# Kernel tuning notes

Measured on AMD Instinct MI355X. Metric: run time of the kernel, lower is better.

## Reference

```python
import jax, jax.numpy as jnp
import numpy as np

D_MODEL, D_STATE, D_CONV, EXPAND = 1024, 16, 4, 2
D_INNER = EXPAND * D_MODEL
B, L = 2, 2048


def setup_inputs() -> dict:
    key = jax.random.key(0)
    ks = jax.random.split(key, 8)
    s = lambda fan: 1.0 / np.sqrt(fan)
    x = jax.random.normal(ks[0], (B, L, D_MODEL), dtype=jnp.float32)
    W_in = jax.random.normal(ks[1], (2 * D_INNER, D_MODEL), dtype=jnp.float32) * s(D_MODEL)
    conv_w = jax.random.normal(ks[2], (D_INNER, 1, D_CONV), dtype=jnp.float32) * s(D_CONV)
    conv_b = jax.random.normal(ks[3], (D_INNER,), dtype=jnp.float32) * 0.01
    A_log = jnp.log(jnp.abs(jax.random.normal(ks[4], (D_INNER, D_STATE), dtype=jnp.float32)) + 1e-4)
    Dp = jnp.ones((D_INNER,), dtype=jnp.float32)
    W_dt = jax.random.normal(ks[5], (D_INNER, D_INNER), dtype=jnp.float32) * s(D_INNER)
    b_dt = jax.random.normal(ks[6], (D_INNER,), dtype=jnp.float32) * 0.01
    W_out = jax.random.normal(ks[7], (D_MODEL, D_INNER), dtype=jnp.float32) * s(D_INNER)
    return {"x": x, "W_in": W_in, "conv_w": conv_w, "conv_b": conv_b,
            "A_log": A_log, "Dp": Dp, "W_dt": W_dt, "b_dt": b_dt, "W_out": W_out}


def _mamba_fwd(x, W_in, conv_w, conv_b, A_log, Dp, W_dt, b_dt, W_out):
    Bsz, Ln, _ = x.shape
    xz = x @ W_in.T                                  # [B, L, 2*d_inner]
    x_proj, z = jnp.split(xz, 2, axis=-1)            # each [B, L, d_inner]
    # depthwise causal conv1d: left-pad d_conv-1 (matches torch pad + [:L] slice)
    xc = jnp.transpose(x_proj, (0, 2, 1))            # [B, C, L]
    xc = jax.lax.conv_general_dilated(
        xc, conv_w, window_strides=(1,), padding=[(D_CONV - 1, 0)],
        dimension_numbers=("NCH", "OIH", "NCH"), feature_group_count=D_INNER)
    xc = xc + conv_b[None, :, None]
    x_act = jax.nn.silu(jnp.transpose(xc, (0, 2, 1)))  # [B, L, d_inner]
    dt = jax.nn.softplus(x_act @ W_dt.T + b_dt)        # [B, L, d_inner]
    A = -jnp.exp(A_log)                                # [d_inner, d_state]

    def step(h, inp):
        xt, dt_t = inp                                 # [B, d_inner] each
        dA = jnp.exp(dt_t[:, :, None] * A[None])       # [B, d_inner, d_state]
        dB = (dt_t * xt)[:, :, None]                   # broadcast over states
        h = dA * h + dB
        y_t = h.sum(axis=-1) + Dp * xt                 # [B, d_inner]
        return h, y_t

    h0 = jnp.zeros((Bsz, D_INNER, D_STATE), dtype=x.dtype)
    xs = (jnp.transpose(x_act, (1, 0, 2)), jnp.transpose(dt, (1, 0, 2)))  # [L, B, d_inner]
    _, ys = jax.lax.scan(step, h0, xs)
    y_ssm = jnp.transpose(ys, (1, 0, 2))               # [B, L, d_inner]
    y_gated = y_ssm * jax.nn.silu(z)
    return y_gated @ W_out.T                           # [B, L, d_model]


def reference(x, W_in, conv_w, conv_b, A_log, Dp, W_dt, b_dt, W_out):
    return _mamba_fwd(x, W_in, conv_w, conv_b, A_log, Dp, W_dt, b_dt, W_out)
```

## Files before the change

### kernel.cpp

```cpp
#include <hip/hip_runtime.h>

#define DMODEL 1024
#define DSTATE 16
#define DCONV  4
#define DINNER 2048
#define BSZ    2
#define LSEQ   2048
#define MTOT   (BSZ * LSEQ)
#define NCH    64
#define LC     (LSEQ / NCH)
#define LOG2E  1.44269504088896f

typedef unsigned short u16;
typedef __attribute__((ext_vector_type(8))) short short8;
typedef __attribute__((ext_vector_type(8))) unsigned short u16x8;
typedef __attribute__((ext_vector_type(4))) float f32x4;

__device__ __forceinline__ float silu_f(float v) {
  return v * __builtin_amdgcn_rcpf(1.f + __builtin_amdgcn_exp2f(-v * LOG2E));
}

__device__ __forceinline__ u16 f2bf(float f) {
  unsigned int u = __float_as_uint(f);
  u += 0x7FFF + ((u >> 16) & 1);
  return (u16)(u >> 16);
}
__device__ __forceinline__ float bf2f(u16 b) { return __uint_as_float(((unsigned int)b) << 16); }

__device__ __forceinline__ void gload_lds16(const u16* g, u16* l) {
  __builtin_amdgcn_global_load_lds((const __attribute__((address_space(1))) unsigned int*)g,
                                   (__attribute__((address_space(3))) unsigned int*)l, 16, 0, 0);
}

__global__ __launch_bounds__(256)
void cast4(const float4* __restrict__ s0, ushort4* __restrict__ d0, int n0,
           const float4* __restrict__ s1, ushort4* __restrict__ d1, int n1,
           const float4* __restrict__ s2, ushort4* __restrict__ d2, int n2,
           const float4* __restrict__ s3, ushort4* __restrict__ d3, int n3) {
  int i = blockIdx.x * 256 + threadIdx.x;
  const float4* s; ushort4* d;
  if (i < n0)                { s = s0; d = d0; }
  else if ((i -= n0) < n1)   { s = s1; d = d1; }
  else if ((i -= n1) < n2)   { s = s2; d = d2; }
  else if ((i -= n2) < n3)   { s = s3; d = d3; }
  else return;
  float4 v = s[i];
  ushort4 o = { f2bf(v.x), f2bf(v.y), f2bf(v.z), f2bf(v.w) };
  d[i] = o;
}

template<int BN, int MODE, int OBF>
__global__ __launch_bounds__(512, 2)
void gemm8p(const u16* __restrict__ A, const u16* __restrict__ Bm,
            const float* __restrict__ bias, void* __restrict__ Cv,
            int M, int N, int K) {
  constexpr int BT  = BN / 32;
  constexpr int TJP = 2;
  constexpr int NPH = BT / TJP;
  constexpr int NBH = BN / 128;
  extern __shared__ __align__(16) u16 smem[];
  u16* As = smem;
  u16* Bs = smem + 2 * 256 * 64;

  const int tid  = threadIdx.x;
  const int lane = tid & 63;
  const int w    = tid >> 6;
  const int quad = lane >> 4;
  const int l16  = lane & 15;
  const int wm   = (w >> 1) * 64;
  const int wn   = (w & 1) * (BN / 2);

  const int nbn = N / BN, nbm = M >> 8;
  const int pid = blockIdx.x;
  const int npg = 4 * nbn;
  const int fm  = (pid / npg) * 4;
  const int gsz = (nbm - fm < 4) ? (nbm - fm) : 4;
  const int bm  = (fm + (pid % gsz)) << 8;
  const int bn  = ((pid % npg) / gsz) * BN;

  const int rseg = lane >> 3;
  const int cd8  = (((lane & 7) ^ rseg) << 3);
  const u16* gA = A  + (size_t)(bm + 16 * w + rseg) * K + cd8;
  const u16* gB = Bm + (size_t)(bn + 16 * w + rseg) * K + cd8;
  u16* lA = &As[(2 * w) << 9];
  u16* lB = &Bs[(2 * w) << 9];
  const int Kmask = K - 1;

  auto stA = [&](int slot, int h, int kt) {
    const size_t go = (size_t)h * 128 * K + ((kt << 6) & Kmask);
    gload_lds16(gA + go,         lA + slot * 16384 + h * 8192);
    gload_lds16(gA + go + 8 * K, lA + slot * 16384 + h * 8192 + 512);
  };
  auto stB = [&](int slot, int h, int kt) {
    const size_t go = (size_t)h * 128 * K + ((kt << 6) & Kmask);
    gload_lds16(gB + go,         lB + slot * (BN * 64) + h * 8192);
    gload_lds16(gB + go + 8 * K, lB + slot * (BN * 64) + h * 8192 + 512);
  };

  int aoff[4][2], boff[BT][2];
#pragma unroll
  for (int t = 0; t < 4; ++t) {
    const int ra = wm + 16 * t + l16;
#pragma unroll
    for (int ks = 0; ks < 2; ++ks)
      aoff[t][ks] = ra * 64 + (((quad + 4 * ks) ^ (ra & 7)) << 3);
  }
#pragma unroll
  for (int tj = 0; tj < BT; ++tj) {
    const int rb = wn + 16 * tj + l16;
#pragma unroll
    for (int ks = 0; ks < 2; ++ks)
      boff[tj][ks] = rb * 64 + (((quad + 4 * ks) ^ (rb & 7)) << 3);
  }

  f32x4 acc[4][BT] = {};
  short8 af[4][2];

#define RD_AF(slot)                                                          \
  { _Pragma("unroll") for (int t = 0; t < 4; ++t)                            \
      _Pragma("unroll") for (int ks = 0; ks < 2; ++ks)                       \
        af[t][ks] = *(const short8*)&As[(slot) * 16384 + aoff[t][ks]]; }

#define VM4 asm volatile("s_waitcnt vmcnt(4)" ::: "memory")
#define NOWAIT ((void)0)

#define PHASE(slot, j, STG, WAIT)                                            \
  {                                                                          \
    if ((j) == 0) RD_AF(slot);                                               \
    short8 bfp[TJP][2];                                                      \
    _Pragma("unroll") for (int jj = 0; jj < TJP; ++jj)                       \
      _Pragma("unroll") for (int ks = 0; ks < 2; ++ks)                       \
        bfp[jj][ks] = *(const short8*)&Bs[(slot) * (BN * 64) +               \
                                          boff[(j) * TJP + jj][ks]];         \
    STG;                                                                     \
    __builtin_amdgcn_s_setprio(1);                                           \
    _Pragma("unroll") for (int ks = 0; ks < 2; ++ks)                         \
      _Pragma("unroll") for (int jj = 0; jj < TJP; ++jj)                     \
        _Pragma("unroll") for (int t = 0; t < 4; ++t)                        \
          acc[t][(j) * TJP + jj] = __builtin_amdgcn_mfma_f32_16x16x32_bf16(  \
              af[t][ks], bfp[jj][ks], acc[t][(j) * TJP + jj], 0, 0, 0);      \
    __builtin_amdgcn_s_setprio(0);                                           \
    asm volatile("s_waitcnt lgkmcnt(0)" ::: "memory");                       \
    WAIT;                                                                    \
    __builtin_amdgcn_s_barrier();                                            \
  }

  stA(0, 0, 0); stA(0, 1, 0);
  stB(0, 0, 0); if (NBH == 2) stB(0, 1, 0);
  stA(1, 0, 1); stA(1, 1, 1);
  VM4;
  __builtin_amdgcn_s_barrier();

  const int niter = K >> 7;
  for (int i = 0; i < niter; ++i) {
    const int tb1 = 2 * i + 1, t2 = 2 * i + 2, t3 = 2 * i + 3;
    if constexpr (NPH == 4) {
      PHASE(0, 0, { stB(1, 0, tb1); },               NOWAIT);
      PHASE(0, 1, { stB(1, 1, tb1); stA(0, 0, t2); }, NOWAIT);
      PHASE(0, 2, { stA(0, 1, t2); },                NOWAIT);
      PHASE(0, 3, {},                                VM4);
      PHASE(1, 0, { stB(0, 0, t2); },                NOWAIT);
      PHASE(1, 1, { stB(0, 1, t2); stA(1, 0, t3); }, NOWAIT);
      PHASE(1, 2, { stA(1, 1, t3); },                NOWAIT);
      PHASE(1, 3, {},                                VM4);
    } else {
      PHASE(0, 0, { stB(1, 0, tb1); },                NOWAIT);
      PHASE(0, 1, { stA(0, 0, t2); stA(0, 1, t2); },  VM4);
      PHASE(1, 0, { stB(0, 0, t2); },                 NOWAIT);
      PHASE(1, 1, { stA(1, 0, t3); stA(1, 1, t3); },  VM4);
    }
  }
#undef PHASE
#undef RD_AF
#undef VM4
#undef NOWAIT

  asm volatile("s_waitcnt vmcnt(0)" ::: "memory");

  const bool dosilu = (MODE == 2) && (bn >= (N >> 1));
#pragma unroll
  for (int t = 0; t < 4; ++t) {
    const int row0 = bm + wm + 16 * t + quad * 4;
#pragma unroll
    for (int tj = 0; tj < BT; ++tj) {
      const int col = bn + wn + 16 * tj + l16;
      const float bv = (MODE == 1) ? bias[col] : 0.f;
#pragma unroll
      for (int i2 = 0; i2 < 4; ++i2) {
        float v = acc[t][tj][i2] + bv;
        if (MODE == 1) v = (v > 20.f) ? v : __logf(1.f + __expf(v));
        if (MODE == 2 && dosilu) v = silu_f(v);
        if (OBF) ((u16*)Cv)[(size_t)(row0 + i2) * N + col] = f2bf(v);
        else     ((float*)Cv)[(size_t)(row0 + i2) * N + col] = v;
      }
    }
  }
}

template<int MODE, int OBF, int BN>
__global__ __launch_bounds__(256)
void hgemm_bk128(const u16* __restrict__ A, const u16* __restrict__ B,
                 const float* __restrict__ bias, void* __restrict__ Cv,
                 int M, int N, int K) {
  constexpr int ASEG = 32;
  constexpr int BSEG = BN / 4;
  constexpr int SPW  = (ASEG + BSEG) / 4;
  constexpr int BT   = BN / 32;
  __shared__ u16 As[128 * 128];
  __shared__ u16 Bs[BN * 128];
  const int tid  = threadIdx.x;
  const int lane = tid & 63;
  const int w    = tid >> 6;
  const int quad = lane >> 4;
  const int l16  = lane & 15;

  const int nbn = N / BN, nbm = M >> 7;
  const int pid = blockIdx.x;
  const int npg = 4 * nbn;
  const int fm  = (pid / npg) * 4;
  const int gsz = (nbm - fm < 4) ? (nbm - fm) : 4;
  const int bm  = (fm + (pid % gsz)) << 7;
  const int bn  = ((pid % npg) / gsz) * BN;

  const int wm = (w & 1) * 64;
  const int wn = (w >> 1) * (BN / 2);

  const int rs4 = lane >> 4;
  const u16* Gp[SPW]; u16* Lp[SPW];
#pragma unroll
  for (int q = 0; q < SPW; ++q) {
    const int g = w * SPW + q;
    if (g < ASEG) {
      const int r  = g * 4 + rs4;
      const int cdk = (lane & 15) ^ (r & 15);
      Gp[q] = A + (size_t)(bm + r) * K + (cdk << 3);
      Lp[q] = &As[g << 9];
    } else {
      const int r  = (g - ASEG) * 4 + rs4;
      const int cdk = (lane & 15) ^ (r & 15);
      Gp[q] = B + (size_t)(bn + r) * K + (cdk << 3);
      Lp[q] = &Bs[(g - ASEG) << 9];
    }
  }

  const short8* Afp[4][4];
  const short8* Bfp[BT][4];
#pragma unroll
  for (int t = 0; t < 4; ++t) {
    const int ra = wm + 16 * t + l16;
#pragma unroll
    for (int ks = 0; ks < 4; ++ks)
      Afp[t][ks] = (const short8*)&As[ra * 128 + (((quad + 4 * ks) ^ (ra & 15)) << 3)];
  }
#pragma unroll
  for (int t = 0; t < BT; ++t) {
    const int rb = wn + 16 * t + l16;
#pragma unroll
    for (int ks = 0; ks < 4; ++ks)
      Bfp[t][ks] = (const short8*)&Bs[rb * 128 + (((quad + 4 * ks) ^ (rb & 15)) << 3)];
  }

  f32x4 acc[4][BT] = {};

  for (int k0 = 0; k0 < K; k0 += 128) {
#pragma unroll
    for (int q = 0; q < SPW; ++q) { gload_lds16(Gp[q], Lp[q]); Gp[q] += 128; }
    __syncthreads();
#pragma unroll
    for (int ks = 0; ks < 4; ++ks) {
      short8 af[4], bf[BT];
#pragma unroll
      for (int t = 0; t < 4; ++t) af[t] = *Afp[t][ks];
#pragma unroll
      for (int t = 0; t < BT; ++t) bf[t] = *Bfp[t][ks];
#pragma unroll
      for (int ti = 0; ti < 4; ++ti)
#pragma unroll
        for (int tj = 0; tj < BT; ++tj)
          acc[ti][tj] = __builtin_amdgcn_mfma_f32_16x16x32_bf16(af[ti], bf[tj],
                                                                acc[ti][tj], 0, 0, 0);
    }
    __syncthreads();
  }

#pragma unroll
  for (int ti = 0; ti < 4; ++ti) {
    const int row0 = bm + wm + 16 * ti + quad * 4;
#pragma unroll
    for (int tj = 0; tj < BT; ++tj) {
      const int col = bn + wn + 16 * tj + l16;
      const float bv = (MODE == 1) ? bias[col] : 0.f;
#pragma unroll
      for (int i = 0; i < 4; ++i) {
        float v = acc[ti][tj][i] + bv;
        if (MODE == 1) v = (v > 20.f) ? v : __logf(1.f + __expf(v));
        if (OBF) ((u16*)Cv)[(size_t)(row0 + i) * N + col] = f2bf(v);
        else     ((float*)Cv)[(size_t)(row0 + i) * N + col] = v;
      }
    }
  }
}

__global__ __launch_bounds__(256)
void conv_silu(const u16* __restrict__ xz, const float* __restrict__ conv_w,
               const float* __restrict__ conv_b, u16* __restrict__ xact) {
  const int i  = blockIdx.x * 256 + threadIdx.x;
  const int ko = i & 255;
  const int t4 = (i >> 8) & (LSEQ / 4 - 1);
  const int b  = i >> 17;
  const int c  = ko << 3;
  const int t0 = t4 << 2;
  float wv[4][8], bias[8];
#pragma unroll
  for (int j = 0; j < 8; ++j) {
    bias[j] = conv_b[c + j];
    const float4 w4 = *(const float4*)(conv_w + (c + j) * DCONV);
    wv[0][j] = w4.x; wv[1][j] = w4.y; wv[2][j] = w4.z; wv[3][j] = w4.w;
  }
  float win[7][8];
#pragma unroll
  for (int r = 0; r < 7; ++r) {
    const int tt = t0 - 3 + r;
    if (tt >= 0) {
      const u16x8 v = *(const u16x8*)(xz + ((size_t)(b * LSEQ + tt) << 12) + c);
#pragma unroll
      for (int j = 0; j < 8; ++j) win[r][j] = bf2f(v[j]);
    } else {
#pragma unroll
      for (int j = 0; j < 8; ++j) win[r][j] = 0.f;
    }
  }
#pragma unroll
  for (int o = 0; o < 4; ++o) {
    u16x8 outv;
#pragma unroll
    for (int j = 0; j < 8; ++j) {
      float a = bias[j];
#pragma unroll
      for (int k = 0; k < 4; ++k) a = fmaf(win[o + k][j], wv[k][j], a);
      outv[j] = f2bf(silu_f(a));
    }
    *(u16x8*)(xact + ((size_t)(b * LSEQ + t0 + o) << 11) + c) = outv;
  }
}


__global__ __launch_bounds__(256, 2)
void scan_pass1(const u16* __restrict__ dtb, const u16* __restrict__ xact,
                const float* __restrict__ A_log,
                u16* __restrict__ hbuf, float* __restrict__ sumdt) {
  const int gid = blockIdx.x * 256 + threadIdx.x;
  const int c  = gid & (DINNER - 1);
  const int ch = (gid >> 11) & (NCH - 1);
  const int b  = gid >> 17;
  float a2[16];
#pragma unroll
  for (int s = 0; s < 16; ++s)
    a2[s] = -__expf(A_log[c * DSTATE + s]) * LOG2E;
  const size_t base = ((size_t)(b * LSEQ + ch * LC) << 11) + c;
  float h[16] = {};
  float sd = 0.f;
  for (int j = 0; j < LC; j += 2) {
    const float dt0 = bf2f(dtb [base + ((size_t)j << 11)]);
    const float xv0 = bf2f(xact[base + ((size_t)j << 11)]);
    const float dt1 = bf2f(dtb [base + ((size_t)(j + 1) << 11)]);
    const float xv1 = bf2f(xact[base + ((size_t)(j + 1) << 11)]);
    const float dx0 = dt0 * xv0, dx1 = dt1 * xv1;
    sd += dt0 + dt1;
#pragma unroll
    for (int s = 0; s < 16; ++s)
      h[s] = fmaf(__builtin_amdgcn_exp2f(dt0 * a2[s]), h[s], dx0);
#pragma unroll
    for (int s = 0; s < 16; ++s)
      h[s] = fmaf(__builtin_amdgcn_exp2f(dt1 * a2[s]), h[s], dx1);
  }
  u16x8* ho = (u16x8*)&hbuf[(((size_t)(b * NCH + ch) * DINNER) + c) << 4];
  u16x8 lo, hi;
#pragma unroll
  for (int s = 0; s < 8; ++s) { lo[s] = f2bf(h[s]); hi[s] = f2bf(h[8 + s]); }
  ho[0] = lo; ho[1] = hi;
  sumdt[(size_t)(b * NCH + ch) * DINNER + c] = sd;
}

__global__ __launch_bounds__(256)
void scan_combine(u16* __restrict__ hbuf, const float* __restrict__ sumdt,
                  const float* __restrict__ A_log) {
  const int gid = blockIdx.x * 256 + threadIdx.x;
  const int s = gid & 15;
  const int c = (gid >> 4) & (DINNER - 1);
  const int b = gid >> 15;
  const float a2 = -__expf(A_log[c * DSTATE + s]) * LOG2E;
  float h = 0.f;
  for (int k = 0; k < NCH; ++k) {
    const size_t o = (((size_t)(b * NCH + k) * DINNER) + c) * 16 + s;
    const float he = bf2f(hbuf[o]);
    const float sd = sumdt[(size_t)(b * NCH + k) * DINNER + c];
    hbuf[o] = f2bf(h);
    h = fmaf(__builtin_amdgcn_exp2f(sd * a2), h, he);
  }
}

__global__ __launch_bounds__(256, 2)
void scan_pass3(const u16* __restrict__ dtb, const u16* __restrict__ xact,
                const u16* __restrict__ xz, const float* __restrict__ A_log,
                const float* __restrict__ Dp, const u16* __restrict__ hbuf,
                u16* __restrict__ yg) {
  const int gid = blockIdx.x * 256 + threadIdx.x;
  const int c  = gid & (DINNER - 1);
  const int ch = (gid >> 11) & (NCH - 1);
  const int b  = gid >> 17;
  float a2[16];
#pragma unroll
  for (int s = 0; s < 16; ++s)
    a2[s] = -__expf(A_log[c * DSTATE + s]) * LOG2E;
  const float dp = Dp[c];
  float h[16];
  const u16x8* hi = (const u16x8*)&hbuf[(((size_t)(b * NCH + ch) * DINNER) + c) << 4];
  const u16x8 vlo = hi[0], vhi = hi[1];
#pragma unroll
  for (int s = 0; s < 8; ++s) { h[s] = bf2f(vlo[s]); h[8 + s] = bf2f(vhi[s]); }
  const size_t base  = ((size_t)(b * LSEQ + ch * LC) << 11) + c;
  const size_t zbase = ((size_t)(b * LSEQ + ch * LC) << 12) + DINNER + c;
  for (int j = 0; j < LC; j += 2) {
    const float dt0 = bf2f(dtb [base + ((size_t)j << 11)]);
    const float xv0 = bf2f(xact[base + ((size_t)j << 11)]);
    const float zv0 = bf2f(xz[zbase + ((size_t)j << 12)]);
    const float dt1 = bf2f(dtb [base + ((size_t)(j + 1) << 11)]);
    const float xv1 = bf2f(xact[base + ((size_t)(j + 1) << 11)]);
    const float zv1 = bf2f(xz[zbase + ((size_t)(j + 1) << 12)]);
    const float dx0 = dt0 * xv0, dx1 = dt1 * xv1;
    float y0 = 0.f, y1 = 0.f;
#pragma unroll
    for (int s = 0; s < 16; ++s) {
      h[s] = fmaf(__builtin_amdgcn_exp2f(dt0 * a2[s]), h[s], dx0);
      y0 += h[s];
    }
#pragma unroll
    for (int s = 0; s < 16; ++s) {
      h[s] = fmaf(__builtin_amdgcn_exp2f(dt1 * a2[s]), h[s], dx1);
      y1 += h[s];
    }
    y0 = fmaf(dp, xv0, y0);
    y1 = fmaf(dp, xv1, y1);
    yg[base + ((size_t)j << 11)]       = f2bf(y0 * zv0);
    yg[base + ((size_t)(j + 1) << 11)] = f2bf(y1 * zv1);
  }
}

extern "C" void kernel_launch(void* const* d_in, const int* in_sizes, int n_in,
                              void* d_out, int out_size, void* d_ws, size_t ws_size,
                              hipStream_t stream) {
  const float* x      = (const float*)d_in[0];
  const float* W_in   = (const float*)d_in[1];
  const float* conv_w = (const float*)d_in[2];
  const float* conv_b = (const float*)d_in[3];
  const float* A_log  = (const float*)d_in[4];
  const float* Dp     = (const float*)d_in[5];
  const float* W_dt   = (const float*)d_in[6];
  const float* b_dt   = (const float*)d_in[7];
  const float* W_out  = (const float*)d_in[8];
  float* out = (float*)d_out;

  u16* xz   = (u16*)d_ws;
  u16* dtb  = xz   + (size_t)MTOT * 2 * DINNER;
  u16* xbf  = dtb  + (size_t)MTOT * DINNER;
  u16* wibf = xbf  + (size_t)MTOT * DMODEL;
  u16* wdbf = wibf + (size_t)2 * DINNER * DMODEL;
  u16* wobf = wdbf + (size_t)DINNER * DINNER;
  u16* xact = wobf + (size_t)DMODEL * DINNER;
  u16* yg   = xact + (size_t)MTOT * DINNER;
  u16* hbuf = yg   + (size_t)MTOT * DINNER;
  float* sumdt = (float*)(hbuf + (size_t)BSZ * NCH * DINNER * 16);

  const dim3 blk(256);

  static bool s_attr = false;
  if (!s_attr) {
    hipFuncSetAttribute(reinterpret_cast<const void*>(&gemm8p<256, 2, 1>),
                        hipFuncAttributeMaxDynamicSharedMemorySize, 131072);
    hipFuncSetAttribute(reinterpret_cast<const void*>(&gemm8p<128, 1, 1>),
                        hipFuncAttributeMaxDynamicSharedMemorySize, 98304);
    s_attr = true;
  }

  const int n0 = MTOT * DMODEL / 4, n1 = 2 * DINNER * DMODEL / 4;
  const int n2 = DINNER * DINNER / 4, n3 = DMODEL * DINNER / 4;
  cast4<<<(n0 + n1 + n2 + n3) / 256, blk, 0, stream>>>(
      (const float4*)x, (ushort4*)xbf, n0,
      (const float4*)W_in, (ushort4*)wibf, n1,
      (const float4*)W_dt, (ushort4*)wdbf, n2,
      (const float4*)W_out, (ushort4*)wobf, n3);

  gemm8p<256, 2, 1><<<(MTOT / 256) * (2 * DINNER / 256), dim3(512), 131072, stream>>>(
      xbf, wibf, nullptr, xz, MTOT, 2 * DINNER, DMODEL);
  conv_silu<<<(BSZ * (LSEQ / 4) * 256) / 256, blk, 0, stream>>>(xz, conv_w, conv_b, xact);
  gemm8p<128, 1, 1><<<(MTOT / 256) * (DINNER / 128), dim3(512), 98304, stream>>>(
      xact, wdbf, b_dt, dtb, MTOT, DINNER, DINNER);
  scan_pass1<<<BSZ * NCH * DINNER / 256, blk, 0, stream>>>(dtb, xact, A_log, hbuf, sumdt);
  scan_combine<<<BSZ * DINNER * 16 / 256, blk, 0, stream>>>(hbuf, sumdt, A_log);
  scan_pass3<<<BSZ * NCH * DINNER / 256, blk, 0, stream>>>(dtb, xact, xz, A_log, Dp, hbuf, yg);
  hgemm_bk128<0, 0, 128><<<(MTOT / 128) * (DMODEL / 128), blk, 0, stream>>>(
      yg, wobf, nullptr, out, MTOT, DMODEL, DINNER);
}
```

Measured before the change: 279.0 us.

## Add triple-buffered 256x128 GEMM kernel for the dt projection

Adds a new gemm3s kernel that uses a three-stage LDS ring buffer with direct global-to-LDS loads issued two K-tiles ahead. Each iteration splits the MFMA work into two halves, interleaving B and A loads between them and raising wave priority during the math. It replaces the gemm8p<128> call for the x_act @ W_dt projection with softplus epilogue. The deeper pipeline is meant to hide global memory latency better, at the cost of 144 KB of shared memory per block, which limits occupancy to one block per CU.

```diff
diff --git a/kernel.cpp b/kernel.cpp
--- a/kernel.cpp
+++ b/kernel.cpp
@@ -197,6 +197,144 @@
   }
 }
 
+template<int MODE>
+__global__ __launch_bounds__(512, 1)
+void gemm3s(const u16* __restrict__ A, const u16* __restrict__ Bm,
+            const float* __restrict__ bias, u16* __restrict__ C,
+            int M, int N, int K) {
+  constexpr int BN = 128;
+  constexpr int BT = 4;
+  extern __shared__ __align__(16) u16 smem[];
+  u16* As = smem;
+  u16* Bs = smem + 3 * 256 * 64;
+
+  const int tid  = threadIdx.x;
+  const int lane = tid & 63;
+  const int w    = tid >> 6;
+  const int quad = lane >> 4;
+  const int l16  = lane & 15;
+  const int wm   = (w >> 1) * 64;
+  const int wn   = (w & 1) * 64;
+
+  const int nbn = N / BN, nbm = M >> 8;
+  const int pid = blockIdx.x;
+  const int npg = 4 * nbn;
+  const int fm  = (pid / npg) * 4;
+  const int gsz = (nbm - fm < 4) ? (nbm - fm) : 4;
+  const int bm  = (fm + (pid % gsz)) << 8;
+  const int bn  = ((pid % npg) / gsz) * BN;
+
+  const int rseg = lane >> 3;
+  const int cd8  = (((lane & 7) ^ rseg) << 3);
+  const u16* gA = A  + (size_t)(bm + 16 * w + rseg) * K + cd8;
+  const u16* gB = Bm + (size_t)(bn + 16 * w + rseg) * K + cd8;
+  u16* lA = &As[(2 * w) << 9];
+  u16* lB = &Bs[(2 * w) << 9];
+  const int Kmask = K - 1;
+
+  auto stA = [&](int slot, int h, int kt) {
+    const size_t go = (size_t)h * 128 * K + ((kt << 6) & Kmask);
+    gload_lds16(gA + go,         lA + slot * 16384 + h * 8192);
+    gload_lds16(gA + go + 8 * K, lA + slot * 16384 + h * 8192 + 512);
+  };
+  auto stB = [&](int slot, int kt) {
+    const size_t go = (kt << 6) & Kmask;
+    gload_lds16(gB + go,         lB + slot * 8192);
+    gload_lds16(gB + go + 8 * K, lB + slot * 8192 + 512);
+  };
+
+  int aoff[4][2], boff[4][2];
+#pragma unroll
+  for (int t = 0; t < 4; ++t) {
+    const int ra = wm + 16 * t + l16;
+    const int rb = wn + 16 * t + l16;
+#pragma unroll
+    for (int ks = 0; ks < 2; ++ks) {
+      aoff[t][ks] = ra * 64 + (((quad + 4 * ks) ^ (ra & 7)) << 3);
+      boff[t][ks] = rb * 64 + (((quad + 4 * ks) ^ (rb & 7)) << 3);
+    }
+  }
+
+  f32x4 acc[4][4] = {};
+  short8 af[4][2];
+
+  stB(0, 0); stA(0, 0, 0); stA(0, 1, 0);
+  stB(1, 1); stA(1, 0, 1); stA(1, 1, 1);
+  asm volatile("s_waitcnt vmcnt(6)" ::: "memory");
+  __builtin_amdgcn_s_barrier();
+
+  int sc = 0, sn = 2;
+  const int nt = K >> 6;
+  for (int t = 0; t < nt; ++t) {
+    const int t2 = t + 2;
+    const int ab = sc * 16384;
+    const int bb = sc * 8192;
+#pragma unroll
+    for (int ti = 0; ti < 4; ++ti)
+#pragma unroll
+      for (int ks = 0; ks < 2; ++ks)
+        af[ti][ks] = *(const short8*)&As[ab + aoff[ti][ks]];
+    short8 bf0[2][2];
+#pragma unroll
+    for (int tj = 0; tj < 2; ++tj)
+#pragma unroll
+      for (int ks = 0; ks < 2; ++ks)
+        bf0[tj][ks] = *(const short8*)&Bs[bb + boff[tj][ks]];
+    stB(sn, t2);
+    __builtin_amdgcn_s_setprio(1);
+#pragma unroll
+    for (int ks = 0; ks < 2; ++ks)
+#pragma unroll
+      for (int tj = 0; tj < 2; ++tj)
+#pragma unroll
+        for (int ti = 0; ti < 4; ++ti)
+          acc[ti][tj] = __builtin_amdgcn_mfma_f32_16x16x32_bf16(
+              af[ti][ks], bf0[tj][ks], acc[ti][tj], 0, 0, 0);
+    __builtin_amdgcn_s_setprio(0);
+    asm volatile("s_waitcnt lgkmcnt(0)" ::: "memory");
+    __builtin_amdgcn_s_barrier();
+    short8 bf1[2][2];
+#pragma unroll
+    for (int tj = 0; tj < 2; ++tj)
+#pragma unroll
+      for (int ks = 0; ks < 2; ++ks)
+        bf1[tj][ks] = *(const short8*)&Bs[bb + boff[2 + tj][ks]];
+    stA(sn, 0, t2); stA(sn, 1, t2);
+    __builtin_amdgcn_s_setprio(1);
+#pragma unroll
+    for (int ks = 0; ks < 2; ++ks)
+#pragma unroll
+      for (int tj = 0; tj < 2; ++tj)
+#pragma unroll
+        for (int ti = 0; ti < 4; ++ti)
+          acc[ti][2 + tj] = __builtin_amdgcn_mfma_f32_16x16x32_bf16(
+              af[ti][ks], bf1[tj][ks], acc[ti][2 + tj], 0, 0, 0);
+    __builtin_amdgcn_s_setprio(0);
+    asm volatile("s_waitcnt lgkmcnt(0)" ::: "memory");
+    asm volatile("s_waitcnt vmcnt(6)" ::: "memory");
+    __builtin_amdgcn_s_barrier();
+    sc = (sc == 2) ? 0 : sc + 1;
+    sn = (sn == 2) ? 0 : sn + 1;
+  }
+  asm volatile("s_waitcnt vmcnt(0)" ::: "memory");
+
+#pragma unroll
+  for (int t = 0; t < 4; ++t) {
+    const int row0 = bm + wm + 16 * t + quad * 4;
+#pragma unroll
+    for (int tj = 0; tj < 4; ++tj) {
+      const int col = bn + wn + 16 * tj + l16;
+      const float bv = (MODE == 1) ? bias[col] : 0.f;
+#pragma unroll
+      for (int i2 = 0; i2 < 4; ++i2) {
+        float v = acc[t][tj][i2] + bv;
+        if (MODE == 1) v = (v > 20.f) ? v : __logf(1.f + __expf(v));
+        C[(size_t)(row0 + i2) * N + col] = f2bf(v);
+      }
+    }
+  }
+}
+
 template<int MODE, int OBF, int BN>
 __global__ __launch_bounds__(256)
 void hgemm_bk128(const u16* __restrict__ A, const u16* __restrict__ B,
@@ -478,8 +616,8 @@
   if (!s_attr) {
     hipFuncSetAttribute(reinterpret_cast<const void*>(&gemm8p<256, 2, 1>),
                         hipFuncAttributeMaxDynamicSharedMemorySize, 131072);
-    hipFuncSetAttribute(reinterpret_cast<const void*>(&gemm8p<128, 1, 1>),
-                        hipFuncAttributeMaxDynamicSharedMemorySize, 98304);
+    hipFuncSetAttribute(reinterpret_cast<const void*>(&gemm3s<1>),
+                        hipFuncAttributeMaxDynamicSharedMemorySize, 147456);
     s_attr = true;
   }
 
@@ -494,7 +632,7 @@
   gemm8p<256, 2, 1><<<(MTOT / 256) * (2 * DINNER / 256), dim3(512), 131072, stream>>>(
       xbf, wibf, nullptr, xz, MTOT, 2 * DINNER, DMODEL);
   conv_silu<<<(BSZ * (LSEQ / 4) * 256) / 256, blk, 0, stream>>>(xz, conv_w, conv_b, xact);
-  gemm8p<128, 1, 1><<<(MTOT / 256) * (DINNER / 128), dim3(512), 98304, stream>>>(
+  gemm3s<1><<<(MTOT / 256) * (DINNER / 128), dim3(512), 147456, stream>>>(
       xact, wdbf, b_dt, dtb, MTOT, DINNER, DINNER);
   scan_pass1<<<BSZ * NCH * DINNER / 256, blk, 0, stream>>>(dtb, xact, A_log, hbuf, sumdt);
   scan_combine<<<BSZ * DINNER * 16 / 256, blk, 0, stream>>>(hbuf, sumdt, A_log);
```

Result: no change. 276.1 us (-1.0%).

## Process two channels per thread in scan passes and parallelize chunk combine

Applied to the files above, without the earlier changes.

Scan pass1 and pass3 now give each thread two adjacent channels, loading dt/x/z as 32-bit pairs and storing y as packed pairs. This halves the number of memory instructions and doubles the independent work per thread, at the cost of twice the register state and half as many threads. The chunk-combine kernel swaps its serial 64-step loop per (b,c,s) for a wavefront-wide shuffle-based associative scan with one lane per chunk. That shortens the serial dependency chain, but launches 64 times more threads, and the hbuf/sumdt reads are strided across lanes.

```diff
diff --git a/kernel.cpp b/kernel.cpp
--- a/kernel.cpp
+++ b/kernel.cpp
@@ -12,6 +12,7 @@
 #define LOG2E  1.44269504088896f
 
 typedef unsigned short u16;
+typedef unsigned int u32;
 typedef __attribute__((ext_vector_type(8))) short short8;
 typedef __attribute__((ext_vector_type(8))) unsigned short u16x8;
 typedef __attribute__((ext_vector_type(4))) float f32x4;
@@ -350,54 +351,66 @@
                 const float* __restrict__ A_log,
                 u16* __restrict__ hbuf, float* __restrict__ sumdt) {
   const int gid = blockIdx.x * 256 + threadIdx.x;
-  const int c  = gid & (DINNER - 1);
-  const int ch = (gid >> 11) & (NCH - 1);
-  const int b  = gid >> 17;
-  float a2[16];
-#pragma unroll
-  for (int s = 0; s < 16; ++s)
-    a2[s] = -__expf(A_log[c * DSTATE + s]) * LOG2E;
+  const int c  = (gid & (DINNER / 2 - 1)) << 1;
+  const int ch = (gid >> 10) & (NCH - 1);
+  const int b  = gid >> 16;
+  float a2[2][16];
+#pragma unroll
+  for (int cc = 0; cc < 2; ++cc)
+#pragma unroll
+    for (int s = 0; s < 16; ++s)
+      a2[cc][s] = -__expf(A_log[(c + cc) * DSTATE + s]) * LOG2E;
   const size_t base = ((size_t)(b * LSEQ + ch * LC) << 11) + c;
-  float h[16] = {};
-  float sd = 0.f;
-  for (int j = 0; j < LC; j += 2) {
-    const float dt0 = bf2f(dtb [base + ((size_t)j << 11)]);
-    const float xv0 = bf2f(xact[base + ((size_t)j << 11)]);
-    const float dt1 = bf2f(dtb [base + ((size_t)(j + 1) << 11)]);
-    const float xv1 = bf2f(xact[base + ((size_t)(j + 1) << 11)]);
-    const float dx0 = dt0 * xv0, dx1 = dt1 * xv1;
-    sd += dt0 + dt1;
+  float h[2][16] = {};
+  float sd0 = 0.f, sd1 = 0.f;
+  for (int j = 0; j < LC; ++j) {
+    const u32 dv = *(const u32*)(dtb  + base + ((size_t)j << 11));
+    const u32 xv = *(const u32*)(xact + base + ((size_t)j << 11));
+    const float dt0 = bf2f((u16)dv), dt1 = bf2f((u16)(dv >> 16));
+    const float x0  = bf2f((u16)xv), x1  = bf2f((u16)(xv >> 16));
+    const float dx0 = dt0 * x0, dx1 = dt1 * x1;
+    sd0 += dt0; sd1 += dt1;
 #pragma unroll
     for (int s = 0; s < 16; ++s)
-      h[s] = fmaf(__builtin_amdgcn_exp2f(dt0 * a2[s]), h[s], dx0);
+      h[0][s] = fmaf(__builtin_amdgcn_exp2f(dt0 * a2[0][s]), h[0][s], dx0);
 #pragma unroll
     for (int s = 0; s < 16; ++s)
-      h[s] = fmaf(__builtin_amdgcn_exp2f(dt1 * a2[s]), h[s], dx1);
+      h[1][s] = fmaf(__builtin_amdgcn_exp2f(dt1 * a2[1][s]), h[1][s], dx1);
   }
   u16x8* ho = (u16x8*)&hbuf[(((size_t)(b * NCH + ch) * DINNER) + c) << 4];
-  u16x8 lo, hi;
-#pragma unroll
-  for (int s = 0; s < 8; ++s) { lo[s] = f2bf(h[s]); hi[s] = f2bf(h[8 + s]); }
-  ho[0] = lo; ho[1] = hi;
-  sumdt[(size_t)(b * NCH + ch) * DINNER + c] = sd;
+#pragma unroll
+  for (int cc = 0; cc < 2; ++cc) {
+    u16x8 lo, hi;
+#pragma unroll
+    for (int s = 0; s < 8; ++s) { lo[s] = f2bf(h[cc][s]); hi[s] = f2bf(h[cc][8 + s]); }
+    ho[2 * cc] = lo; ho[2 * cc + 1] = hi;
+  }
+  *(float2*)&sumdt[(size_t)(b * NCH + ch) * DINNER + c] = make_float2(sd0, sd1);
 }
 
 __global__ __launch_bounds__(256)
 void scan_combine(u16* __restrict__ hbuf, const float* __restrict__ sumdt,
                   const float* __restrict__ A_log) {
-  const int gid = blockIdx.x * 256 + threadIdx.x;
-  const int s = gid & 15;
-  const int c = (gid >> 4) & (DINNER - 1);
-  const int b = gid >> 15;
+  const int wid  = (blockIdx.x * 256 + threadIdx.x) >> 6;
+  const int lane = threadIdx.x & 63;
+  const int s = wid & 15;
+  const int c = (wid >> 4) & (DINNER - 1);
+  const int b = wid >> 15;
   const float a2 = -__expf(A_log[c * DSTATE + s]) * LOG2E;
-  float h = 0.f;
-  for (int k = 0; k < NCH; ++k) {
-    const size_t o = (((size_t)(b * NCH + k) * DINNER) + c) * 16 + s;
-    const float he = bf2f(hbuf[o]);
-    const float sd = sumdt[(size_t)(b * NCH + k) * DINNER + c];
-    hbuf[o] = f2bf(h);
-    h = fmaf(__builtin_amdgcn_exp2f(sd * a2), h, he);
-  }
+  const size_t o = (((size_t)(b * NCH + lane) * DINNER) + c) * 16 + s;
+  const float he = bf2f(hbuf[o]);
+  const float sd = sumdt[(size_t)(b * NCH + lane) * DINNER + c];
+  float a  = __builtin_amdgcn_exp2f(sd * a2);
+  float bb = he;
+#pragma unroll
+  for (int off = 1; off < 64; off <<= 1) {
+    const float pa = __shfl_up(a, off, 64);
+    const float pb = __shfl_up(bb, off, 64);
+    if (lane >= off) { bb = fmaf(a, pb, bb); a *= pa; }
+  }
+  float hs = __shfl_up(bb, 1, 64);
+  if (lane == 0) hs = 0.f;
+  hbuf[o] = f2bf(hs);
 }
 
 __global__ __launch_bounds__(256, 2)
@@ -406,44 +419,48 @@
                 const float* __restrict__ Dp, const u16* __restrict__ hbuf,
                 u16* __restrict__ yg) {
   const int gid = blockIdx.x * 256 + threadIdx.x;
-  const int c  = gid & (DINNER - 1);
-  const int ch = (gid >> 11) & (NCH - 1);
-  const int b  = gid >> 17;
-  float a2[16];
-#pragma unroll
-  for (int s = 0; s < 16; ++s)
-    a2[s] = -__expf(A_log[c * DSTATE + s]) * LOG2E;
-  const float dp = Dp[c];
-  float h[16];
+  const int c  = (gid & (DINNER / 2 - 1)) << 1;
+  const int ch = (gid >> 10) & (NCH - 1);
+  const int b  = gid >> 16;
+  float a2[2][16];
+#pragma unroll
+  for (int cc = 0; cc < 2; ++cc)
+#pragma unroll
+    for (int s = 0; s < 16; ++s)
+      a2[cc][s] = -__expf(A_log[(c + cc) * DSTATE + s]) * LOG2E;
+  const float dp0 = Dp[c], dp1 = Dp[c + 1];
+  float h[2][16];
   const u16x8* hi = (const u16x8*)&hbuf[(((size_t)(b * NCH + ch) * DINNER) + c) << 4];
-  const u16x8 vlo = hi[0], vhi = hi[1];
-#pragma unroll
-  for (int s = 0; s < 8; ++s) { h[s] = bf2f(vlo[s]); h[8 + s] = bf2f(vhi[s]); }
+#pragma unroll
+  for (int cc = 0; cc < 2; ++cc) {
+    const u16x8 vlo = hi[2 * cc], vhi = hi[2 * cc + 1];
+#pragma unroll
+    for (int s = 0; s < 8; ++s) { h[cc][s] = bf2f(vlo[s]); h[cc][8 + s] = bf2f(vhi[s]); }
+  }
   const size_t base  = ((size_t)(b * LSEQ + ch * LC) << 11) + c;
   const size_t zbase = ((size_t)(b * LSEQ + ch * LC) << 12) + DINNER + c;
-  for (int j = 0; j < LC; j += 2) {
-    const float dt0 = bf2f(dtb [base + ((size_t)j << 11)]);
-    const float xv0 = bf2f(xact[base + ((size_t)j << 11)]);
-    const float zv0 = bf2f(xz[zbase + ((size_t)j << 12)]);
-    const float dt1 = bf2f(dtb [base + ((size_t)(j + 1) << 11)]);
-    const float xv1 = bf2f(xact[base + ((size_t)(j + 1) << 11)]);
-    const float zv1 = bf2f(xz[zbase + ((size_t)(j + 1) << 12)]);
-    const float dx0 = dt0 * xv0, dx1 = dt1 * xv1;
+  for (int j = 0; j < LC; ++j) {
+    const u32 dv = *(const u32*)(dtb  + base + ((size_t)j << 11));
+    const u32 xv = *(const u32*)(xact + base + ((size_t)j << 11));
+    const u32 zv = *(const u32*)(xz   + zbase + ((size_t)j << 12));
+    const float dt0 = bf2f((u16)dv), dt1 = bf2f((u16)(dv >> 16));
+    const float x0  = bf2f((u16)xv), x1  = bf2f((u16)(xv >> 16));
+    const float z0  = bf2f((u16)zv), z1  = bf2f((u16)(zv >> 16));
+    const float dx0 = dt0 * x0, dx1 = dt1 * x1;
     float y0 = 0.f, y1 = 0.f;
 #pragma unroll
     for (int s = 0; s < 16; ++s) {
-      h[s] = fmaf(__builtin_amdgcn_exp2f(dt0 * a2[s]), h[s], dx0);
-      y0 += h[s];
+      h[0][s] = fmaf(__builtin_amdgcn_exp2f(dt0 * a2[0][s]), h[0][s], dx0);
+      y0 += h[0][s];
     }
 #pragma unroll
     for (int s = 0; s < 16; ++s) {
-      h[s] = fmaf(__builtin_amdgcn_exp2f(dt1 * a2[s]), h[s], dx1);
-      y1 += h[s];
-    }
-    y0 = fmaf(dp, xv0, y0);
-    y1 = fmaf(dp, xv1, y1);
-    yg[base + ((size_t)j << 11)]       = f2bf(y0 * zv0);
-    yg[base + ((size_t)(j + 1) << 11)] = f2bf(y1 * zv1);
+      h[1][s] = fmaf(__builtin_amdgcn_exp2f(dt1 * a2[1][s]), h[1][s], dx1);
+      y1 += h[1][s];
+    }
+    y0 = fmaf(dp0, x0, y0) * z0;
+    y1 = fmaf(dp1, x1, y1) * z1;
+    *(u32*)(yg + base + ((size_t)j << 11)) = (u32)f2bf(y0) | ((u32)f2bf(y1) << 16);
   }
 }
 
@@ -496,9 +513,9 @@
   conv_silu<<<(BSZ * (LSEQ / 4) * 256) / 256, blk, 0, stream>>>(xz, conv_w, conv_b, xact);
   gemm8p<128, 1, 1><<<(MTOT / 256) * (DINNER / 128), dim3(512), 98304, stream>>>(
       xact, wdbf, b_dt, dtb, MTOT, DINNER, DINNER);
-  scan_pass1<<<BSZ * NCH * DINNER / 256, blk, 0, stream>>>(dtb, xact, A_log, hbuf, sumdt);
-  scan_combine<<<BSZ * DINNER * 16 / 256, blk, 0, stream>>>(hbuf, sumdt, A_log);
-  scan_pass3<<<BSZ * NCH * DINNER / 256, blk, 0, stream>>>(dtb, xact, xz, A_log, Dp, hbuf, yg);
+  scan_pass1<<<BSZ * NCH * DINNER / 2 / 256, blk, 0, stream>>>(dtb, xact, A_log, hbuf, sumdt);
+  scan_combine<<<BSZ * DINNER * DSTATE * 64 / 256, blk, 0, stream>>>(hbuf, sumdt, A_log);
+  scan_pass3<<<BSZ * NCH * DINNER / 2 / 256, blk, 0, stream>>>(dtb, xact, xz, A_log, Dp, hbuf, yg);
   hgemm_bk128<0, 0, 128><<<(MTOT / 128) * (DMODEL / 128), blk, 0, stream>>>(
       yg, wobf, nullptr, out, MTOT, DMODEL, DINNER);
 }
```

After: 314.7 us (median of 2 runs). +12.8%, slower.
